# Optimization experiments

Hardware: AMD Instinct MI355X
Metric: run time of the kernel (lower is better)

Reference implementation:

```python
import jax, jax.numpy as jnp
import numpy as np

B, N, F_DIM, R_DIM = 4, 512, 64, 128


def _pair_indices(n):
    # Same order as the original python double loop: i outer, j inner, skip i==j.
    ii, jj = np.meshgrid(np.arange(n), np.arange(n), indexing='ij')
    mask = ii != jj
    return jnp.asarray(ii[mask]), jnp.asarray(jj[mask])  # each [N*(N-1)]


def setup_inputs() -> dict:
    key = jax.random.key(0)
    ks = jax.random.split(key, 7)
    s1 = 1.0 / np.sqrt(2 * F_DIM)
    s2 = 1.0 / np.sqrt(R_DIM)
    return {
        'features': jax.random.normal(ks[0], (B, N, F_DIM), dtype=jnp.float32),
        'W1': jax.random.uniform(ks[1], (2 * F_DIM, R_DIM), jnp.float32, -s1, s1),
        'b1': jax.random.uniform(ks[2], (R_DIM,), jnp.float32, -s1, s1),
        'W2': jax.random.uniform(ks[3], (R_DIM, R_DIM), jnp.float32, -s2, s2),
        'b2': jax.random.uniform(ks[4], (R_DIM,), jnp.float32, -s2, s2),
        'W3': jax.random.uniform(ks[5], (R_DIM, 1), jnp.float32, -s2, s2),
        'b3': jax.random.uniform(ks[6], (1,), jnp.float32, -s2, s2),
    }


def reference(features, W1, b1, W2, b2, W3, b3):
    n = features.shape[1]
    idx_i, idx_j = _pair_indices(n)
    # Gather all ordered pairs (i != j): [B, P, 2F]
    pair = jnp.concatenate([features[:, idx_i, :], features[:, idx_j, :]], axis=-1)
    h = jax.nn.relu(jnp.einsum('bpf,fr->bpr', pair, W1) + b1)
    h = jax.nn.relu(jnp.einsum('bpr,rs->bps', h, W2) + b2)
    out = jnp.einsum('bpr,ro->bpo', h, W3) + b3  # [B, P, 1]
    return out
```

## Files before the change

### kernel.cpp

```cpp
#include <hip/hip_runtime.h>
#include <stdint.h>

#define B_ 4
#define N_ 512
#define F_ 64
#define R_ 128
#define PPI 511
#define TI 4
#define TJ 128
#define VSTR 136

typedef _Float16 f16x8 __attribute__((ext_vector_type(8)));
typedef _Float16 f16x2 __attribute__((ext_vector_type(2)));
typedef float f32x4 __attribute__((ext_vector_type(4)));

__device__ __forceinline__ uint16_t f16bits(float x) {
  return __builtin_bit_cast(uint16_t, (_Float16)x);
}
__device__ __forceinline__ f16x2 cvt_pk(float a, float b) {
  return __builtin_bit_cast(f16x2, __builtin_amdgcn_cvt_pkrtz(a, b));
}

__global__ __launch_bounds__(256) void prep_all(
    const float* __restrict__ feat, const float* __restrict__ W1,
    const float* __restrict__ b1, const float* __restrict__ W2,
    uint16_t* __restrict__ U, uint16_t* __restrict__ V, uint16_t* __restrict__ w2f) {
  if (blockIdx.x >= 256) {
    const int d = (blockIdx.x - 256) * 256 + threadIdx.x;
    const int jj = d & 7, lane = (d >> 3) & 63, tc = d >> 9;
    const int c = tc & 3, t = tc >> 2;
    const int rr = 32 * c + (lane >> 4) * 8 + jj;
    const int s = 16 * t + (lane & 15);
    w2f[d] = f16bits(W2[rr * R_ + s]);
    return;
  }
  __shared__ float fs[8][F_];
  const int row0 = blockIdx.x * 8;
  const int tid = threadIdx.x;
  for (int l = tid; l < 8 * F_; l += 256) fs[l >> 6][l & 63] = feat[row0 * F_ + l];
  __syncthreads();
  const int r = tid & 127, rh = tid >> 7;
  float aU[4], aV[4];
  const float bias = b1[r];
#pragma unroll
  for (int ii = 0; ii < 4; ++ii) { aU[ii] = bias; aV[ii] = 0.f; }
  for (int f = 0; f < F_; ++f) {
    const float wa = W1[f * R_ + r];
    const float wb = W1[(F_ + f) * R_ + r];
#pragma unroll
    for (int ii = 0; ii < 4; ++ii) {
      aU[ii] = fmaf(fs[rh * 4 + ii][f], wa, aU[ii]);
      aV[ii] = fmaf(fs[rh * 4 + ii][f], wb, aV[ii]);
    }
  }
#pragma unroll
  for (int ii = 0; ii < 4; ++ii) {
    const int row = row0 + rh * 4 + ii;
    U[row * R_ + r] = f16bits(aU[ii]);
    V[row * R_ + r] = f16bits(aV[ii]);
  }
}

__global__ __launch_bounds__(256, 2) void relnet_main(
    const uint16_t* __restrict__ U, const uint16_t* __restrict__ V,
    const uint16_t* __restrict__ w2f, const float* __restrict__ b2,
    const float* __restrict__ W3, const float* __restrict__ b3,
    float* __restrict__ out) {
  __shared__ __align__(16) uint16_t Vs[TJ * VSTR];
  __shared__ __align__(16) uint16_t Us[TI * VSTR];

  const int bid = blockIdx.x;
  const int jb = bid & 3, ib = (bid >> 2) & 127, b = bid >> 9;
  const int i0 = ib * TI, j0 = jb * TJ;
  const int tid = threadIdx.x;

  {
    const uint4* sv = (const uint4*)(V + (b * N_ + j0) * R_);
    for (int l = tid; l < TJ * 16; l += 256) {
      const int row = l >> 4, seg = l & 15;
      *(uint4*)&Vs[row * VSTR + seg * 8] = sv[row * 16 + seg];
    }
    const uint4* su = (const uint4*)(U + (b * N_ + i0) * R_);
    for (int l = tid; l < TI * 16; l += 256) {
      const int row = l >> 4, seg = l & 15;
      *(uint4*)&Us[row * VSTR + seg * 8] = su[row * 16 + seg];
    }
  }

  const int lane = tid & 63, wave = tid >> 6;
  const int quad = lane >> 4, l4 = lane & 15;
  const int i = i0 + wave;

  f16x8 w2r[8][4];
#pragma unroll
  for (int t = 0; t < 8; ++t)
#pragma unroll
    for (int c = 0; c < 4; ++c) {
      const uint4 w = *(const uint4*)(w2f + ((size_t)((t * 4 + c) * 64 + lane)) * 8);
      w2r[t][c] = __builtin_bit_cast(f16x8, w);
    }

  f16x2 b2p[8][2], w3p[8][2];
#pragma unroll
  for (int t = 0; t < 8; ++t)
#pragma unroll
    for (int h = 0; h < 2; ++h) {
      const int s0 = 16 * t + 4 * quad + 2 * h;
      b2p[t][h] = (f16x2){(_Float16)b2[s0], (_Float16)b2[s0 + 1]};
      w3p[t][h] = (f16x2){(_Float16)W3[s0], (_Float16)W3[s0 + 1]};
    }
  const float b3v = b3[0];

  __syncthreads();

  f16x8 uf[4];
#pragma unroll
  for (int c = 0; c < 4; ++c)
    uf[c] = __builtin_bit_cast(f16x8, *(const uint4*)&Us[wave * VSTR + c * 32 + quad * 8]);

  const f16x8 z8 = {};
  const f16x2 z2 = {};

#pragma unroll 2
  for (int jt = 0; jt < 8; ++jt) {
    f16x8 hb[4];
#pragma unroll
    for (int c = 0; c < 4; ++c) {
      const uint4 v = *(const uint4*)&Vs[(jt * 16 + l4) * VSTR + c * 32 + quad * 8];
      hb[c] = __builtin_elementwise_max(__builtin_bit_cast(f16x8, v) + uf[c], z8);
    }

    f32x4 acc[8];
#pragma unroll
    for (int t = 0; t < 8; ++t) acc[t] = (f32x4){0.f, 0.f, 0.f, 0.f};
#pragma unroll
    for (int c = 0; c < 4; ++c)
#pragma unroll
      for (int t = 0; t < 8; ++t)
        acc[t] = __builtin_amdgcn_mfma_f32_16x16x32_f16(w2r[t][c], hb[c], acc[t], 0, 0, 0);

    float t0 = 0.f, t1 = 0.f, t2 = 0.f, t3 = 0.f;
#pragma unroll
    for (int t = 0; t < 8; t += 2) {
      f16x2 p0 = cvt_pk(acc[t][0], acc[t][1]);
      f16x2 p1 = cvt_pk(acc[t][2], acc[t][3]);
      p0 = __builtin_elementwise_max(p0 + b2p[t][0], z2);
      p1 = __builtin_elementwise_max(p1 + b2p[t][1], z2);
      t0 = __builtin_amdgcn_fdot2(p0, w3p[t][0], t0, false);
      t1 = __builtin_amdgcn_fdot2(p1, w3p[t][1], t1, false);
      f16x2 q0 = cvt_pk(acc[t + 1][0], acc[t + 1][1]);
      f16x2 q1 = cvt_pk(acc[t + 1][2], acc[t + 1][3]);
      q0 = __builtin_elementwise_max(q0 + b2p[t + 1][0], z2);
      q1 = __builtin_elementwise_max(q1 + b2p[t + 1][1], z2);
      t2 = __builtin_amdgcn_fdot2(q0, w3p[t + 1][0], t2, false);
      t3 = __builtin_amdgcn_fdot2(q1, w3p[t + 1][1], t3, false);
    }
    float tot = (t0 + t1) + (t2 + t3);
    tot += __shfl_xor(tot, 16, 64);
    tot += __shfl_xor(tot, 32, 64);

    if (lane < 16) {
      const int j = j0 + jt * 16 + lane;
      if (j != i) {
        const int p = (b * N_ + i) * PPI + (j < i ? j : j - 1);
        out[p] = tot + b3v;
      }
    }
  }
}

extern "C" void kernel_launch(void* const* d_in, const int* in_sizes, int n_in,
                              void* d_out, int out_size, void* d_ws, size_t ws_size,
                              hipStream_t stream) {
  const float* feat = (const float*)d_in[0];
  const float* W1 = (const float*)d_in[1];
  const float* b1 = (const float*)d_in[2];
  const float* W2 = (const float*)d_in[3];
  const float* b2 = (const float*)d_in[4];
  const float* W3 = (const float*)d_in[5];
  const float* b3 = (const float*)d_in[6];

  uint16_t* U = (uint16_t*)d_ws;
  uint16_t* V = U + (size_t)B_ * N_ * R_;
  uint16_t* w2f = V + (size_t)B_ * N_ * R_;

  prep_all<<<256 + 64, 256, 0, stream>>>(feat, W1, b1, W2, U, V, w2f);
  relnet_main<<<B_ * (N_ / TI) * (N_ / TJ), 256, 0, stream>>>(U, V, w2f, b2, W3, b3,
                                                              (float*)d_out);
}
```

Measured before the change: 107.3 us.

## Split W2 output columns across wave pairs to cut registers, reduce via LDS

Each block now handles 2 i-rows instead of 4, and the two waves per row each hold half of W2 (4 column tiles instead of 8). This roughly halves the W2 register footprint per wave, and launch bounds are raised so more blocks can fit per CU. Partial dot products go to LDS and are summed after a barrier before the output is written. In exchange, twice as many blocks each reload the same V tile, and the kernel gains an extra shared-memory reduction and barrier; the prep loop also gets an unroll pragma.

```diff
diff --git a/kernel.cpp b/kernel.cpp
--- a/kernel.cpp
+++ b/kernel.cpp
@@ -6,7 +6,6 @@
 #define F_ 64
 #define R_ 128
 #define PPI 511
-#define TI 4
 #define TJ 128
 #define VSTR 136
 
@@ -44,6 +43,7 @@
   const float bias = b1[r];
 #pragma unroll
   for (int ii = 0; ii < 4; ++ii) { aU[ii] = bias; aV[ii] = 0.f; }
+#pragma unroll 4
   for (int f = 0; f < F_; ++f) {
     const float wa = W1[f * R_ + r];
     const float wb = W1[(F_ + f) * R_ + r];
@@ -61,17 +61,17 @@
   }
 }
 
-__global__ __launch_bounds__(256, 2) void relnet_main(
+__global__ __launch_bounds__(256, 3) void relnet_main(
     const uint16_t* __restrict__ U, const uint16_t* __restrict__ V,
     const uint16_t* __restrict__ w2f, const float* __restrict__ b2,
     const float* __restrict__ W3, const float* __restrict__ b3,
     float* __restrict__ out) {
   __shared__ __align__(16) uint16_t Vs[TJ * VSTR];
-  __shared__ __align__(16) uint16_t Us[TI * VSTR];
+  __shared__ float pl[4][2][2][8][16];
 
   const int bid = blockIdx.x;
-  const int jb = bid & 3, ib = (bid >> 2) & 127, b = bid >> 9;
-  const int i0 = ib * TI, j0 = jb * TJ;
+  const int jb = bid & 3, ib = (bid >> 2) & 255, b = bid >> 10;
+  const int i0 = ib * 2, j0 = jb * TJ;
   const int tid = threadIdx.x;
 
   {
@@ -80,46 +80,45 @@
       const int row = l >> 4, seg = l & 15;
       *(uint4*)&Vs[row * VSTR + seg * 8] = sv[row * 16 + seg];
     }
-    const uint4* su = (const uint4*)(U + (b * N_ + i0) * R_);
-    for (int l = tid; l < TI * 16; l += 256) {
-      const int row = l >> 4, seg = l & 15;
-      *(uint4*)&Us[row * VSTR + seg * 8] = su[row * 16 + seg];
-    }
   }
 
   const int lane = tid & 63, wave = tid >> 6;
   const int quad = lane >> 4, l4 = lane & 15;
-  const int i = i0 + wave;
+  const int il = wave >> 1, th = wave & 1;
+  const int i = i0 + il;
 
-  f16x8 w2r[8][4];
+  f16x8 w2r[4][4];
 #pragma unroll
-  for (int t = 0; t < 8; ++t)
+  for (int tp = 0; tp < 4; ++tp)
 #pragma unroll
     for (int c = 0; c < 4; ++c) {
+      const int t = th * 4 + tp;
       const uint4 w = *(const uint4*)(w2f + ((size_t)((t * 4 + c) * 64 + lane)) * 8);
-      w2r[t][c] = __builtin_bit_cast(f16x8, w);
+      w2r[tp][c] = __builtin_bit_cast(f16x8, w);
     }
 
-  f16x2 b2p[8][2], w3p[8][2];
+  f16x2 b2p[4][2], w3p[4][2];
 #pragma unroll
-  for (int t = 0; t < 8; ++t)
+  for (int tp = 0; tp < 4; ++tp)
 #pragma unroll
     for (int h = 0; h < 2; ++h) {
-      const int s0 = 16 * t + 4 * quad + 2 * h;
-      b2p[t][h] = (f16x2){(_Float16)b2[s0], (_Float16)b2[s0 + 1]};
-      w3p[t][h] = (f16x2){(_Float16)W3[s0], (_Float16)W3[s0 + 1]};
+      const int s0 = 16 * (th * 4 + tp) + 4 * quad + 2 * h;
+      b2p[tp][h] = (f16x2){(_Float16)b2[s0], (_Float16)b2[s0 + 1]};
+      w3p[tp][h] = (f16x2){(_Float16)W3[s0], (_Float16)W3[s0 + 1]};
     }
-  const float b3v = b3[0];
-
-  __syncthreads();
 
   f16x8 uf[4];
 #pragma unroll
   for (int c = 0; c < 4; ++c)
-    uf[c] = __builtin_bit_cast(f16x8, *(const uint4*)&Us[wave * VSTR + c * 32 + quad * 8]);
+    uf[c] = __builtin_bit_cast(f16x8,
+        *(const uint4*)(U + (size_t)(b * N_ + i) * R_ + c * 32 + quad * 8));
 
   const f16x8 z8 = {};
   const f16x2 z2 = {};
+
+  __syncthreads();
+
+  float part[8];
 
 #pragma unroll 2
   for (int jt = 0; jt < 8; ++jt) {
@@ -130,41 +129,51 @@
       hb[c] = __builtin_elementwise_max(__builtin_bit_cast(f16x8, v) + uf[c], z8);
     }
 
-    f32x4 acc[8];
+    f32x4 acc[4];
 #pragma unroll
-    for (int t = 0; t < 8; ++t) acc[t] = (f32x4){0.f, 0.f, 0.f, 0.f};
+    for (int tp = 0; tp < 4; ++tp) acc[tp] = (f32x4){0.f, 0.f, 0.f, 0.f};
 #pragma unroll
     for (int c = 0; c < 4; ++c)
 #pragma unroll
-      for (int t = 0; t < 8; ++t)
-        acc[t] = __builtin_amdgcn_mfma_f32_16x16x32_f16(w2r[t][c], hb[c], acc[t], 0, 0, 0);
+      for (int tp = 0; tp < 4; ++tp)
+        acc[tp] = __builtin_amdgcn_mfma_f32_16x16x32_f16(w2r[tp][c], hb[c], acc[tp], 0, 0, 0);
 
     float t0 = 0.f, t1 = 0.f, t2 = 0.f, t3 = 0.f;
 #pragma unroll
-    for (int t = 0; t < 8; t += 2) {
-      f16x2 p0 = cvt_pk(acc[t][0], acc[t][1]);
-      f16x2 p1 = cvt_pk(acc[t][2], acc[t][3]);
-      p0 = __builtin_elementwise_max(p0 + b2p[t][0], z2);
-      p1 = __builtin_elementwise_max(p1 + b2p[t][1], z2);
-      t0 = __builtin_amdgcn_fdot2(p0, w3p[t][0], t0, false);
-      t1 = __builtin_amdgcn_fdot2(p1, w3p[t][1], t1, false);
-      f16x2 q0 = cvt_pk(acc[t + 1][0], acc[t + 1][1]);
-      f16x2 q1 = cvt_pk(acc[t + 1][2], acc[t + 1][3]);
-      q0 = __builtin_elementwise_max(q0 + b2p[t + 1][0], z2);
-      q1 = __builtin_elementwise_max(q1 + b2p[t + 1][1], z2);
-      t2 = __builtin_amdgcn_fdot2(q0, w3p[t + 1][0], t2, false);
-      t3 = __builtin_amdgcn_fdot2(q1, w3p[t + 1][1], t3, false);
+    for (int tp = 0; tp < 4; tp += 2) {
+      f16x2 p0 = cvt_pk(acc[tp][0], acc[tp][1]);
+      f16x2 p1 = cvt_pk(acc[tp][2], acc[tp][3]);
+      p0 = __builtin_elementwise_max(p0 + b2p[tp][0], z2);
+      p1 = __builtin_elementwise_max(p1 + b2p[tp][1], z2);
+      t0 = __builtin_amdgcn_fdot2(p0, w3p[tp][0], t0, false);
+      t1 = __builtin_amdgcn_fdot2(p1, w3p[tp][1], t1, false);
+      f16x2 q0 = cvt_pk(acc[tp + 1][0], acc[tp + 1][1]);
+      f16x2 q1 = cvt_pk(acc[tp + 1][2], acc[tp + 1][3]);
+      q0 = __builtin_elementwise_max(q0 + b2p[tp + 1][0], z2);
+      q1 = __builtin_elementwise_max(q1 + b2p[tp + 1][1], z2);
+      t2 = __builtin_amdgcn_fdot2(q0, w3p[tp + 1][0], t2, false);
+      t3 = __builtin_amdgcn_fdot2(q1, w3p[tp + 1][1], t3, false);
     }
-    float tot = (t0 + t1) + (t2 + t3);
-    tot += __shfl_xor(tot, 16, 64);
-    tot += __shfl_xor(tot, 32, 64);
+    part[jt] = (t0 + t1) + (t2 + t3);
+  }
 
-    if (lane < 16) {
-      const int j = j0 + jt * 16 + lane;
-      if (j != i) {
-        const int p = (b * N_ + i) * PPI + (j < i ? j : j - 1);
-        out[p] = tot + b3v;
-      }
+#pragma unroll
+  for (int jt = 0; jt < 8; ++jt) pl[quad][th][il][jt][l4] = part[jt];
+
+  __syncthreads();
+
+  {
+    const int ril = tid >> 7, rjt = (tid >> 4) & 7, rl4 = tid & 15;
+    float sum = b3[0];
+#pragma unroll
+    for (int q = 0; q < 4; ++q)
+#pragma unroll
+      for (int h = 0; h < 2; ++h) sum += pl[q][h][ril][rjt][rl4];
+    const int ri = i0 + ril;
+    const int j = j0 + rjt * 16 + rl4;
+    if (j != ri) {
+      const int p = (b * N_ + ri) * PPI + (j < ri ? j : j - 1);
+      out[p] = sum;
     }
   }
 }
@@ -185,6 +194,6 @@
   uint16_t* w2f = V + (size_t)B_ * N_ * R_;
 
   prep_all<<<256 + 64, 256, 0, stream>>>(feat, W1, b1, W2, U, V, w2f);
-  relnet_main<<<B_ * (N_ / TI) * (N_ / TJ), 256, 0, stream>>>(U, V, w2f, b2, W3, b3,
-                                                              (float*)d_out);
+  relnet_main<<<B_ * (N_ / 2) * (N_ / TJ), 256, 0, stream>>>(U, V, w2f, b2, W3, b3,
+                                                             (float*)d_out);
 }
```

New measurement: 110.0 us. 2.5% more time.
